# Performance work log

Measured on AMD Instinct MI355X. Metric: run time of the kernel, lower is better.

Reference implementation:

```python
import jax, jax.numpy as jnp
import numpy as np

B, E, N, F = 8, 2048, 2048, 128

def setup_inputs() -> dict:
    key = jax.random.key(0)
    k1, k2, k3, k4 = jax.random.split(key, 4)
    node_embeddings = jax.random.normal(k1, (B, N, F), dtype=jnp.float32)
    adj = jax.random.randint(k2, (B, E, N), -1, 3).astype(jnp.float32)
    W = jax.random.normal(k3, (F, F), dtype=jnp.float32) * (1.0 / np.sqrt(F))
    b = jax.random.normal(k4, (F,), dtype=jnp.float32) * 0.01
    return {"node_embeddings": node_embeddings, "adj": adj, "W": W, "b": b}

def reference(node_embeddings, adj, W, b):
    # adj_target: 1 where adj == -1, else 0
    adj_target = (adj == -1).astype(node_embeddings.dtype)          # [B, E, N]
    norm = jnp.sum(adj_target, axis=-1, keepdims=True)               # [B, E, 1]
    norm = jnp.where(norm == 0, 1.0, norm)
    # masked-mean aggregation of neighbor vertices into hyperedges
    message_vertex = jnp.matmul(adj_target, node_embeddings) / norm  # [B, E, F]
    # linear (torch Linear: x @ W.T + b) + relu
    hyperedge_embeddings = jax.nn.relu(jnp.matmul(message_vertex, W.T) + b)
    return hyperedge_embeddings
```

## Files before the change

### kernel.cpp

```cpp
#include <hip/hip_runtime.h>
#include <hip/hip_bf16.h>

#define B_ 8
#define E_ 2048
#define N_ 2048
#define F_ 128

#define BM 64
#define MT 4
#define BK 64
#define MP 136

using bf16x8 = __bf16 __attribute__((ext_vector_type(8)));
using fx4    = float __attribute__((ext_vector_type(4)));

__global__ __launch_bounds__(256) void prep_all(const float* __restrict__ node,
                                                const float* __restrict__ W,
                                                __bf16* __restrict__ nodeT,
                                                __bf16* __restrict__ Wb) {
    const int bid = blockIdx.x;
    const int t   = threadIdx.x;

    if (bid < 512) {
        const int b  = bid & 7;
        const int n0 = (bid >> 3) * 32;
        const int f  = t & 127;
        const int nb = n0 + (t >> 7) * 16;
        const float* src = node + ((size_t)b * N_ + nb) * F_ + f;
        __bf16 h[16];
#pragma unroll
        for (int i = 0; i < 16; ++i)
            h[i] = (__bf16)src[(size_t)i * F_];
        __bf16* dst = nodeT + ((size_t)b * F_ + f) * N_ + nb;
        *(uint4*)&dst[0] = *(const uint4*)&h[0];
        *(uint4*)&dst[8] = *(const uint4*)&h[8];
    } else {
        int idx = (bid - 512) * 256 + t;
        float4 v = *(const float4*)&W[idx * 4];
        __bf16 o[4] = {(__bf16)v.x, (__bf16)v.y, (__bf16)v.z, (__bf16)v.w};
        *(uint2*)&Wb[idx * 4] = *(const uint2*)o;
    }
}

__global__ __launch_bounds__(256, 1) void v2h_main(const float* __restrict__ adj,
                                                   const __bf16* __restrict__ nodeT,
                                                   const __bf16* __restrict__ Wb,
                                                   const float* __restrict__ bias,
                                                   float* __restrict__ out) {
    __shared__ __align__(16) __bf16 Bs[2][128][64];
    __shared__ __align__(16) unsigned long long Abits[2][64];
    __shared__ __align__(16) float normS[BM];
    __shared__ __align__(16) __bf16 Ms[BM * MP];

    const int t    = threadIdx.x;
    const int bid  = blockIdx.x;
    const int b    = bid & 7;
    const int e0   = (bid >> 3) * BM;
    const int w    = t >> 6;
    const int lane = t & 63;
    const int l15  = lane & 15;
    const int quad = lane >> 4;

    const int ar   = lane >> 2;
    const int acs  = lane & 3;
    const int arow = w * 16 + ar;
    const float* aPtr = adj + ((size_t)b * E_ + e0 + arow) * N_ + acs * 16;

    const __bf16* nTB = nodeT + (size_t)b * F_ * N_;

    auto issue_dma = [&](int k0, int buf) {
#pragma unroll
        for (int p = 0; p < 4; ++p) {
            int idx = t + 256 * p;
            int f   = idx >> 3;
            int sl  = idx & 7;
            int g   = sl ^ (f & 7);
            const __bf16* src = nTB + (size_t)f * N_ + k0 + g * 8;
            __bf16* dst = &Bs[buf][0][0] + (size_t)(w * 64 + 256 * p) * 8;
            __builtin_amdgcn_global_load_lds(
                (const __attribute__((address_space(1))) void*)src,
                (__attribute__((address_space(3))) void*)dst, 16, 0, 0);
        }
    };

    auto cvt16 = [](float4 v0, float4 v1, float4 v2, float4 v3) -> unsigned {
        unsigned m = 0;
        m |= (v0.x == -1.f) ? 1u     : 0u;
        m |= (v0.y == -1.f) ? 2u     : 0u;
        m |= (v0.z == -1.f) ? 4u     : 0u;
        m |= (v0.w == -1.f) ? 8u     : 0u;
        m |= (v1.x == -1.f) ? 16u    : 0u;
        m |= (v1.y == -1.f) ? 32u    : 0u;
        m |= (v1.z == -1.f) ? 64u    : 0u;
        m |= (v1.w == -1.f) ? 128u   : 0u;
        m |= (v2.x == -1.f) ? 256u   : 0u;
        m |= (v2.y == -1.f) ? 512u   : 0u;
        m |= (v2.z == -1.f) ? 1024u  : 0u;
        m |= (v2.w == -1.f) ? 2048u  : 0u;
        m |= (v3.x == -1.f) ? 4096u  : 0u;
        m |= (v3.y == -1.f) ? 8192u  : 0u;
        m |= (v3.z == -1.f) ? 16384u : 0u;
        m |= (v3.w == -1.f) ? 32768u : 0u;
        return m;
    };

    auto unpack = [](unsigned byte) -> bf16x8 {
        union { unsigned u[4]; bf16x8 v; } r;
        r.u[0] = ((byte &   1u) ? 0x3F80u : 0u) | ((byte &   2u) ? 0x3F800000u : 0u);
        r.u[1] = ((byte &   4u) ? 0x3F80u : 0u) | ((byte &   8u) ? 0x3F800000u : 0u);
        r.u[2] = ((byte &  16u) ? 0x3F80u : 0u) | ((byte &  32u) ? 0x3F800000u : 0u);
        r.u[3] = ((byte &  64u) ? 0x3F80u : 0u) | ((byte & 128u) ? 0x3F800000u : 0u);
        return r.v;
    };

    fx4 acc[MT][2] = {};
    int cnt = 0;

    float4 a0 = *(const float4*)(aPtr + 0);
    float4 a1 = *(const float4*)(aPtr + 4);
    float4 a2 = *(const float4*)(aPtr + 8);
    float4 a3 = *(const float4*)(aPtr + 12);
    issue_dma(0, 0);
    {
        unsigned bits = cvt16(a0, a1, a2, a3);
        ((unsigned short*)&Abits[0][arow])[acs] = (unsigned short)bits;
        cnt += __popc(bits);
    }
    a0 = *(const float4*)(aPtr + BK + 0);
    a1 = *(const float4*)(aPtr + BK + 4);
    a2 = *(const float4*)(aPtr + BK + 8);
    a3 = *(const float4*)(aPtr + BK + 12);

#pragma unroll
    for (int m = 0; m < 32; ++m) {
        const int buf = m & 1;
        __syncthreads();

        if (m < 31)
            issue_dma((m + 1) * BK, buf ^ 1);
        if (m < 31) {
            unsigned bits = cvt16(a0, a1, a2, a3);
            ((unsigned short*)&Abits[buf ^ 1][arow])[acs] = (unsigned short)bits;
            cnt += __popc(bits);
        }
        if (m < 30) {
            const float* ap = aPtr + (m + 2) * BK;
            a0 = *(const float4*)(ap + 0);
            a1 = *(const float4*)(ap + 4);
            a2 = *(const float4*)(ap + 8);
            a3 = *(const float4*)(ap + 12);
        }

        bf16x8 af0[MT], af1[MT];
#pragma unroll
        for (int mt = 0; mt < MT; ++mt) {
            unsigned long long v = Abits[buf][mt * 16 + l15];
            unsigned lo = (unsigned)v, hi = (unsigned)(v >> 32);
            af0[mt] = unpack((lo >> (8 * quad)) & 255u);
            af1[mt] = unpack((hi >> (8 * quad)) & 255u);
        }

#pragma unroll
        for (int ft = 0; ft < 2; ++ft) {
            int f  = w * 32 + ft * 16 + l15;
            int q0 = quad ^ (f & 7);
            int q1 = (4 + quad) ^ (f & 7);
            bf16x8 b0 = *(const bf16x8*)&Bs[buf][f][q0 * 8];
#pragma unroll
            for (int mt = 0; mt < MT; ++mt)
                acc[mt][ft] = __builtin_amdgcn_mfma_f32_16x16x32_bf16(af0[mt], b0, acc[mt][ft], 0, 0, 0);
            bf16x8 b1 = *(const bf16x8*)&Bs[buf][f][q1 * 8];
#pragma unroll
            for (int mt = 0; mt < MT; ++mt)
                acc[mt][ft] = __builtin_amdgcn_mfma_f32_16x16x32_bf16(af1[mt], b1, acc[mt][ft], 0, 0, 0);
        }
    }

    {
        float c = (float)cnt;
        c += __shfl_xor(c, 1);
        c += __shfl_xor(c, 2);
        if (acs == 0)
            normS[arow] = 1.f / fmaxf(c, 1.f);
    }
    __syncthreads();

    const int rbase = quad * 4;
    float4 rn[MT];
#pragma unroll
    for (int mt = 0; mt < MT; ++mt)
        rn[mt] = *(const float4*)&normS[mt * 16 + rbase];

#pragma unroll
    for (int ft = 0; ft < 2; ++ft) {
        int fcol = w * 32 + ft * 16 + l15;
#pragma unroll
        for (int mt = 0; mt < MT; ++mt) {
            const float* rr = (const float*)&rn[mt];
#pragma unroll
            for (int r = 0; r < 4; ++r)
                Ms[(mt * 16 + rbase + r) * MP + fcol] = (__bf16)(acc[mt][ft][r] * rr[r]);
        }
    }
    __syncthreads();

    fx4 acc2[MT][2] = {};
#pragma unroll
    for (int ks = 0; ks < 4; ++ks) {
        bf16x8 afm[MT];
#pragma unroll
        for (int mt = 0; mt < MT; ++mt)
            afm[mt] = *(const bf16x8*)&Ms[(mt * 16 + l15) * MP + ks * 32 + quad * 8];
#pragma unroll
        for (int gt = 0; gt < 2; ++gt) {
            int g = w * 32 + gt * 16 + l15;
            bf16x8 wfr = *(const bf16x8*)&Wb[(size_t)g * F_ + ks * 32 + quad * 8];
#pragma unroll
            for (int mt = 0; mt < MT; ++mt)
                acc2[mt][gt] = __builtin_amdgcn_mfma_f32_16x16x32_bf16(afm[mt], wfr, acc2[mt][gt], 0, 0, 0);
        }
    }

#pragma unroll
    for (int gt = 0; gt < 2; ++gt) {
        int g = w * 32 + gt * 16 + l15;
        float bb = bias[g];
#pragma unroll
        for (int mt = 0; mt < MT; ++mt) {
#pragma unroll
            for (int r = 0; r < 4; ++r) {
                int e = e0 + mt * 16 + rbase + r;
                float v = acc2[mt][gt][r] + bb;
                out[((size_t)b * E_ + e) * F_ + g] = fmaxf(v, 0.f);
            }
        }
    }
}

extern "C" void kernel_launch(void* const* d_in, const int* in_sizes, int n_in,
                              void* d_out, int out_size, void* d_ws, size_t ws_size,
                              hipStream_t stream) {
    const float* node = (const float*)d_in[0];
    const float* adj  = (const float*)d_in[1];
    const float* W    = (const float*)d_in[2];
    const float* bias = (const float*)d_in[3];
    float* out = (float*)d_out;

    char* ws = (char*)d_ws;
    __bf16* nodeT = (__bf16*)ws;
    __bf16* Wb    = (__bf16*)(ws + 8 * 1024 * 1024);

    prep_all<<<528, 256, 0, stream>>>(node, W, nodeT, Wb);
    v2h_main<<<256, 256, 0, stream>>>(adj, nodeT, Wb, bias, out);
}
```

Measured before the change: 213.0 us.

## Deepen adjacency register prefetch to two stages with partial vmcnt barriers

Keeps two K-tiles of fp32 adjacency loads in flight in registers instead of one. The plain __syncthreads is replaced by inline s_waitcnt vmcnt(4) plus s_barrier, so the newest global loads are not drained at each barrier, and sched_barrier fences stop the compiler from reordering around them. The goal is to hide HBM latency on the adjacency stream, which is the dominant memory traffic. In exchange it uses more VGPRs, and the hand-counted vmcnt relies on exactly how many loads issue_dma emits.

```diff
diff --git a/kernel.cpp b/kernel.cpp
--- a/kernel.cpp
+++ b/kernel.cpp
@@ -116,39 +116,53 @@
     fx4 acc[MT][2] = {};
     int cnt = 0;
 
-    float4 a0 = *(const float4*)(aPtr + 0);
-    float4 a1 = *(const float4*)(aPtr + 4);
-    float4 a2 = *(const float4*)(aPtr + 8);
-    float4 a3 = *(const float4*)(aPtr + 12);
+    float4 aS[2][4];
+    aS[0][0] = *(const float4*)(aPtr + 0);
+    aS[0][1] = *(const float4*)(aPtr + 4);
+    aS[0][2] = *(const float4*)(aPtr + 8);
+    aS[0][3] = *(const float4*)(aPtr + 12);
+    aS[1][0] = *(const float4*)(aPtr + BK + 0);
+    aS[1][1] = *(const float4*)(aPtr + BK + 4);
+    aS[1][2] = *(const float4*)(aPtr + BK + 8);
+    aS[1][3] = *(const float4*)(aPtr + BK + 12);
     issue_dma(0, 0);
+    __builtin_amdgcn_sched_barrier(0);
     {
-        unsigned bits = cvt16(a0, a1, a2, a3);
+        unsigned bits = cvt16(aS[0][0], aS[0][1], aS[0][2], aS[0][3]);
         ((unsigned short*)&Abits[0][arow])[acs] = (unsigned short)bits;
         cnt += __popc(bits);
     }
-    a0 = *(const float4*)(aPtr + BK + 0);
-    a1 = *(const float4*)(aPtr + BK + 4);
-    a2 = *(const float4*)(aPtr + BK + 8);
-    a3 = *(const float4*)(aPtr + BK + 12);
+    aS[0][0] = *(const float4*)(aPtr + 2 * BK + 0);
+    aS[0][1] = *(const float4*)(aPtr + 2 * BK + 4);
+    aS[0][2] = *(const float4*)(aPtr + 2 * BK + 8);
+    aS[0][3] = *(const float4*)(aPtr + 2 * BK + 12);
 
 #pragma unroll
     for (int m = 0; m < 32; ++m) {
         const int buf = m & 1;
-        __syncthreads();
+
+        if (m >= 30)
+            asm volatile("s_waitcnt vmcnt(0) lgkmcnt(0)\n\ts_barrier" ::: "memory");
+        else
+            asm volatile("s_waitcnt vmcnt(4) lgkmcnt(0)\n\ts_barrier" ::: "memory");
+        __builtin_amdgcn_sched_barrier(0);
 
         if (m < 31)
             issue_dma((m + 1) * BK, buf ^ 1);
+        __builtin_amdgcn_sched_barrier(0);
+
         if (m < 31) {
-            unsigned bits = cvt16(a0, a1, a2, a3);
+            const float4* s = aS[(m + 1) & 1];
+            unsigned bits = cvt16(s[0], s[1], s[2], s[3]);
             ((unsigned short*)&Abits[buf ^ 1][arow])[acs] = (unsigned short)bits;
             cnt += __popc(bits);
         }
-        if (m < 30) {
-            const float* ap = aPtr + (m + 2) * BK;
-            a0 = *(const float4*)(ap + 0);
-            a1 = *(const float4*)(ap + 4);
-            a2 = *(const float4*)(ap + 8);
-            a3 = *(const float4*)(ap + 12);
+        if (m < 29) {
+            const float* ap = aPtr + (m + 3) * BK;
+            aS[(m + 1) & 1][0] = *(const float4*)(ap + 0);
+            aS[(m + 1) & 1][1] = *(const float4*)(ap + 4);
+            aS[(m + 1) & 1][2] = *(const float4*)(ap + 8);
+            aS[(m + 1) & 1][3] = *(const float4*)(ap + 12);
         }
 
         bf16x8 af0[MT], af1[MT];
```

Measured after the change: 215.7 us. No clear change (+1.3%).
